# Optimization experiments

Hardware: AMD Instinct MI355X
Metric: run time of the kernel (lower is better)

## Reference

```python
import jax, jax.numpy as jnp
import numpy as np

B, N, DIM, HEADS = 8, 512, 512, 16
MAX_DIST, NG = 128, 32
RBF_STOP = 20.0
EPS = 1e-5


def _ln(x, g, b):
    m = jnp.mean(x, axis=-1, keepdims=True)
    v = jnp.mean((x - m) ** 2, axis=-1, keepdims=True)
    return (x - m) * jax.lax.rsqrt(v + EPS) * g + b


def setup_inputs() -> dict:
    key = jax.random.key(0)
    ks = jax.random.split(key, 12)
    d = DIM
    s = 0.02
    return {
        "x": jax.random.normal(ks[0], (B * N, d), jnp.float32),
        "dist_matrix": jax.random.randint(ks[1], (B, N, N), 0, MAX_DIST, jnp.int32),
        "dist_3d": jax.random.uniform(ks[2], (B, N, N), jnp.float32) * RBF_STOP,
        "norm1_g": jnp.ones((d,), jnp.float32),
        "norm1_b": jnp.zeros((d,), jnp.float32),
        "in_proj_w": jax.random.normal(ks[3], (3 * d, d), jnp.float32) * s,
        "in_proj_b": jnp.zeros((3 * d,), jnp.float32),
        "out_proj_w": jax.random.normal(ks[4], (d, d), jnp.float32) * s,
        "out_proj_b": jnp.zeros((d,), jnp.float32),
        "dist_emb": jax.random.normal(ks[5], (MAX_DIST, HEADS), jnp.float32) * s,
        "rbf_w": jax.random.normal(ks[6], (HEADS, NG), jnp.float32) * s,
        "rbf_b": jnp.zeros((HEADS,), jnp.float32),
        "norm2_g": jnp.ones((d,), jnp.float32),
        "norm2_b": jnp.zeros((d,), jnp.float32),
        "ffn_w1": jax.random.normal(ks[7], (4 * d, d), jnp.float32) * s,
        "ffn_b1": jnp.zeros((4 * d,), jnp.float32),
        "ffn_w2": jax.random.normal(ks[8], (d, 4 * d), jnp.float32) * s,
        "ffn_b2": jnp.zeros((d,), jnp.float32),
        "batch": jnp.repeat(jnp.arange(B, dtype=jnp.int32), N),
    }


def reference(x, dist_matrix, dist_3d, norm1_g, norm1_b, in_proj_w, in_proj_b,
              out_proj_w, out_proj_b, dist_emb, rbf_w, rbf_b, norm2_g, norm2_b,
              ffn_w1, ffn_b1, ffn_w2, ffn_b2, batch):
    b, n = dist_matrix.shape[0], dist_matrix.shape[1]
    d = x.shape[-1]
    dh = d // HEADS
    # equal-size graphs -> to_dense_batch is a reshape, mask all-true
    xd = x.reshape(b, n, d)

    # additive attention bias: shortest-path-distance embedding + RBF projection
    dc = jnp.clip(dist_matrix, 0, MAX_DIST - 1)
    bias_spd = dist_emb[dc]                                  # [b, n, n, H]
    offset = jnp.linspace(0.0, RBF_STOP, NG, dtype=jnp.float32)
    coeff = -0.5 / (RBF_STOP / (NG - 1)) ** 2
    rbf = jnp.exp(coeff * (dist_3d[..., None] - offset) ** 2)  # [b, n, n, NG]
    bias_3d = rbf @ rbf_w.T + rbf_b                          # [b, n, n, H]
    bias = jnp.transpose(bias_spd + bias_3d, (0, 3, 1, 2))   # [b, H, n, n]

    # multi-head attention (pre-norm residual, as in source)
    h = _ln(xd, norm1_g, norm1_b)
    qkv = h @ in_proj_w.T + in_proj_b
    q, k, v = jnp.split(qkv, 3, axis=-1)
    q = q.reshape(b, n, HEADS, dh).transpose(0, 2, 1, 3)
    k = k.reshape(b, n, HEADS, dh).transpose(0, 2, 1, 3)
    v = v.reshape(b, n, HEADS, dh).transpose(0, 2, 1, 3)
    scores = jnp.einsum('bhqd,bhkd->bhqk', q, k) / jnp.sqrt(jnp.float32(dh)) + bias
    attn = jax.nn.softmax(scores, axis=-1)
    ctx = jnp.einsum('bhqk,bhkd->bhqd', attn, v)
    ctx = ctx.transpose(0, 2, 1, 3).reshape(b, n, d)
    attn_out = ctx @ out_proj_w.T + out_proj_b
    h = h + attn_out

    # FFN (dropout inactive at eval)
    h2 = _ln(h, norm2_g, norm2_b)
    ff = jax.nn.gelu(h2 @ ffn_w1.T + ffn_b1, approximate=False) @ ffn_w2.T + ffn_b2
    h = h + ff
    return h.reshape(b * n, d)
```

## Files before the change

### kernel.cpp

```cpp
#include <hip/hip_runtime.h>
#include <hip/hip_bf16.h>
#include <math.h>

#define BB 8
#define NN 512
#define DD 512
#define NH 16
#define DH 32
#define TD 1536
#define NG 32
#define MAXD 128

typedef __attribute__((ext_vector_type(8))) short bf16x8;
typedef __attribute__((ext_vector_type(4))) float f32x4;

__device__ inline short f2bf(float x) {
    __hip_bfloat16 h = __float2bfloat16(x);
    return *reinterpret_cast<short*>(&h);
}
__device__ inline float bf2f(short x) {
    union { unsigned u; float f; } c;
    c.u = ((unsigned)(unsigned short)x) << 16;
    return c.f;
}

__device__ inline void gld_lds16(const void* g, void* l) {
    __builtin_amdgcn_global_load_lds(
        (const __attribute__((address_space(1))) unsigned int*)g,
        (__attribute__((address_space(3))) unsigned int*)l, 16, 0, 0);
}

__global__ __launch_bounds__(256) void cvt_weights(
    const float* __restrict__ s0, const float* __restrict__ s1,
    const float* __restrict__ s2, const float* __restrict__ s3,
    short* __restrict__ d0, short* __restrict__ d1,
    short* __restrict__ d2, short* __restrict__ d3,
    const float* __restrict__ rbfw, const float* __restrict__ rbfb,
    short* __restrict__ Tg,
    int n0, int n1, int n2, int n3) {
    if (blockIdx.y == 4) {
        if (blockIdx.x != 0) return;
        const float STEP  = 20.0f / 31.0f;
        const float COEFF = -0.5f / (STEP * STEP);
        for (int idx = threadIdx.x; idx < 130 * 16; idx += 256) {
            const int i = idx >> 4, h = idx & 15;
            const float x = fminf((float)i, 128.0f) * (20.0f / 128.0f);
            float acc = rbfb[h];
#pragma unroll
            for (int g = 0; g < NG; g++) {
                const float t = x - (float)g * STEP;
                acc += __expf(COEFF * t * t) * rbfw[h * NG + g];
            }
            Tg[idx] = f2bf(acc);
        }
        return;
    }
    const float* s; short* d; int n;
    switch (blockIdx.y) {
        case 0: s = s0; d = d0; n = n0; break;
        case 1: s = s1; d = d1; n = n1; break;
        case 2: s = s2; d = d2; n = n2; break;
        default: s = s3; d = d3; n = n3; break;
    }
    const int i = (blockIdx.x * 256 + threadIdx.x) * 4;
    if (i >= n) return;
    const float4 v = *(const float4*)(s + i);
    short4 o;
    o.x = f2bf(v.x); o.y = f2bf(v.y); o.z = f2bf(v.z); o.w = f2bf(v.w);
    *(short4*)(d + i) = o;
}

__global__ __launch_bounds__(256) void ln_kernel(const float* __restrict__ x,
                                                 const float* __restrict__ g,
                                                 const float* __restrict__ b,
                                                 short* __restrict__ out_bf,
                                                 float* __restrict__ out_f) {
    const int row = blockIdx.x;
    const int tid = threadIdx.x;
    const int wave = tid >> 6, lane = tid & 63;
    const float* xr = x + (size_t)row * DD;
    const float v0 = xr[tid], v1 = xr[tid + 256];
    float s = v0 + v1, q = v0 * v0 + v1 * v1;
#pragma unroll
    for (int m = 1; m < 64; m <<= 1) { s += __shfl_xor(s, m); q += __shfl_xor(q, m); }
    __shared__ float ps[8];
    if (lane == 0) { ps[wave] = s; ps[wave + 4] = q; }
    __syncthreads();
    s = ps[0] + ps[1] + ps[2] + ps[3];
    q = ps[4] + ps[5] + ps[6] + ps[7];
    const float mean = s * (1.0f / DD);
    const float var  = q * (1.0f / DD) - mean * mean;
    const float rs   = rsqrtf(var + 1e-5f);
    const float o0 = (v0 - mean) * rs * g[tid] + b[tid];
    const float o1 = (v1 - mean) * rs * g[tid + 256] + b[tid + 256];
    out_bf[(size_t)row * DD + tid]       = f2bf(o0);
    out_bf[(size_t)row * DD + tid + 256] = f2bf(o1);
    if (out_f) {
        out_f[(size_t)row * DD + tid]       = o0;
        out_f[(size_t)row * DD + tid + 256] = o1;
    }
}

template <int TM, bool GELU, bool RES, int OUT>
__global__ __launch_bounds__(256) void gemm_bf16(
    const short* __restrict__ A, const short* __restrict__ Bw,
    const float* __restrict__ bias, const float* __restrict__ res,
    void* __restrict__ Cout, int M, int Nout, int K) {
    const int MI = TM / 32;
    const int bm = blockIdx.y * TM;
    const int bn = blockIdx.x * 128;
    const int tid  = threadIdx.x;
    const int wave = tid >> 6;
    const int lane = tid & 63;
    const int l16  = lane & 15;
    const int quad = lane >> 4;
    const int wr = (wave >> 1) * (TM / 2);
    const int wc = (wave & 1) * 64;

    __shared__ short As[2][TM * 32];
    __shared__ short Bs[2][128 * 32];

    f32x4 acc[MI][4];
#pragma unroll
    for (int i = 0; i < MI; i++)
#pragma unroll
        for (int j = 0; j < 4; j++) acc[i][j] = (f32x4){0.f, 0.f, 0.f, 0.f};

    auto stage = [&](int buf, int k0) {
        const short* Ab = A + (size_t)bm * K + k0;
        const short* Bb = Bw + (size_t)bn * K + k0;
#pragma unroll
        for (int j = 0; j < TM / 64; j++) {
            const int idx = j * 256 + wave * 64 + lane;
            gld_lds16(Ab + (size_t)(idx >> 2) * K + (idx & 3) * 8,
                      &As[buf][(size_t)(j * 256 + wave * 64) * 8]);
        }
#pragma unroll
        for (int j = 0; j < 2; j++) {
            const int idx = j * 256 + wave * 64 + lane;
            gld_lds16(Bb + (size_t)(idx >> 2) * K + (idx & 3) * 8,
                      &Bs[buf][(size_t)(j * 256 + wave * 64) * 8]);
        }
    };
    auto compute = [&](int buf) {
        bf16x8 af[MI], bfr[4];
#pragma unroll
        for (int i = 0; i < MI; i++)
            af[i] = *(const bf16x8*)&As[buf][(wr + i * 16 + l16) * 32 + quad * 8];
#pragma unroll
        for (int j = 0; j < 4; j++)
            bfr[j] = *(const bf16x8*)&Bs[buf][(wc + j * 16 + l16) * 32 + quad * 8];
#pragma unroll
        for (int i = 0; i < MI; i++)
#pragma unroll
            for (int j = 0; j < 4; j++)
                acc[i][j] = __builtin_amdgcn_mfma_f32_16x16x32_bf16(af[i], bfr[j], acc[i][j], 0, 0, 0);
    };

    stage(0, 0);
    __syncthreads();
    int cur = 0;
    for (int k0 = 32; k0 < K; k0 += 32) {
        stage(cur ^ 1, k0);
        compute(cur);
        __syncthreads();
        cur ^= 1;
    }
    compute(cur);

#pragma unroll
    for (int i = 0; i < MI; i++) {
#pragma unroll
        for (int r = 0; r < 4; r++) {
            const int row = bm + wr + i * 16 + quad * 4 + r;
#pragma unroll
            for (int j = 0; j < 4; j++) {
                const int col = bn + wc + j * 16 + l16;
                float v = acc[i][j][r] + bias[col];
                if (GELU) v = 0.5f * v * (1.0f + erff(v * 0.70710678118654752f));
                if (RES)  v += res[(size_t)row * Nout + col];
                if (OUT == 1) ((short*)Cout)[(size_t)row * Nout + col] = f2bf(v);
                else          ((float*)Cout)[(size_t)row * Nout + col] = v;
            }
        }
    }
}

__global__ __launch_bounds__(512) void attn_mfma(
    const short* __restrict__ qkv,
    const int* __restrict__ dist,
    const float* __restrict__ dist3d,
    const float* __restrict__ demb,
    const short* __restrict__ Tg,
    float* __restrict__ O_part,
    float* __restrict__ l_part)
{
    const int blk  = blockIdx.x;
    const int b    = blk & 7;
    const int t3   = blk >> 3;
    const int part = t3 % 3;
    const int q0   = (t3 / 3) * 16;
    const int tid  = threadIdx.x;
    const int wave = tid >> 6;
    const int lane = tid & 63;
    const int l16  = lane & 15;
    const int quad = lane >> 4;

    __shared__ short Kc[NH * 16 * 32];
    __shared__ short Vc[NH * 16 * 32];
    __shared__ short Pb[8 * 16 * 34];
    __shared__ short Tt[130 * 18];
    __shared__ short Db[128 * 18];

    for (int i = tid; i < 8 * 16 * 34; i += 512) Pb[i] = 0;
    for (int i = tid; i < 130 * 16; i += 512) Tt[(i >> 4) * 18 + (i & 15)] = Tg[i];
    for (int i = tid; i < 128 * 16; i += 512) Db[(i >> 4) * 18 + (i & 15)] = f2bf(demb[i]);

    const float scale = 0.17677669529663687f;
    bf16x8 qf[2];
#pragma unroll
    for (int h = 0; h < 2; h++) {
        const int hh = wave * 2 + h;
        qf[h] = *(const bf16x8*)(qkv + (size_t)(b * NN + q0 + l16) * TD + hh * DH + quad * 8);
    }

    f32x4 O[2][2];
    float lsum[2][4];
#pragma unroll
    for (int h = 0; h < 2; h++) {
#pragma unroll
        for (int tt = 0; tt < 2; tt++) O[h][tt] = (f32x4){0.f, 0.f, 0.f, 0.f};
#pragma unroll
        for (int r = 0; r < 4; r++) lsum[h][r] = 0.f;
    }

    const int cbeg = part * 11;
    const int cend = (part == 2) ? 32 : cbeg + 11;

    for (int c = cbeg; c < cend; c++) {
        const int k0 = c * 16;
        __syncthreads();
#pragma unroll
        for (int l = 0; l < 4; l++) {
            const int idxb = l * 512 + wave * 64;
            const int idx  = idxb + lane;
            const int kk2  = idx & 1023;
            const int h = kk2 >> 6, k = (kk2 >> 2) & 15, c4 = kk2 & 3;
            const short* src = qkv + (size_t)(b * NN + k0 + k) * TD +
                               DD * (1 + (l >> 1)) + h * 32 + c4 * 8;
            short* dstb = (l < 2 ? (short*)Kc : (short*)Vc) + (size_t)(idxb & 1023) * 8;
            gld_lds16(src, dstb);
        }
        float biasr[2][4];
        {
            const int hh0 = wave * 2, hh1 = hh0 + 1;
#pragma unroll
            for (int r = 0; r < 4; r++) {
                const size_t off = ((size_t)(b * NN) + q0 + quad * 4 + r) * NN + k0 + l16;
                int dc = dist[off];
                dc = min(max(dc, 0), MAXD - 1);
                const float x = dist3d[off] * 6.4f;
                int ii = (int)x; ii = min(ii, 127);
                const float fr = x - (float)ii;
                const float t00 = bf2f(Tt[ii * 18 + hh0]), t01 = bf2f(Tt[ii * 18 + 18 + hh0]);
                const float t10 = bf2f(Tt[ii * 18 + hh1]), t11 = bf2f(Tt[ii * 18 + 18 + hh1]);
                biasr[0][r] = bf2f(Db[dc * 18 + hh0]) + t00 + (t01 - t00) * fr;
                biasr[1][r] = bf2f(Db[dc * 18 + hh1]) + t10 + (t11 - t10) * fr;
            }
        }
        __syncthreads();
#pragma unroll
        for (int h = 0; h < 2; h++) {
            const int hh = wave * 2 + h;
            const bf16x8 kf = *(const bf16x8*)&Kc[hh * 512 + l16 * 32 + quad * 8];
            f32x4 s = __builtin_amdgcn_mfma_f32_16x16x32_bf16(
                qf[h], kf, (f32x4){0.f, 0.f, 0.f, 0.f}, 0, 0, 0);
            float pv[4];
#pragma unroll
            for (int r = 0; r < 4; r++) {
                float sv = s[r] * scale + biasr[h][r];
                sv = fminf(sv, 20.f);
                pv[r] = __expf(sv);
                lsum[h][r] += pv[r];
                Pb[wave * 544 + (quad * 4 + r) * 34 + l16] = f2bf(pv[r]);
            }
            const bf16x8 pf = *(const bf16x8*)&Pb[wave * 544 + l16 * 34 + quad * 8];
#pragma unroll
            for (int tt = 0; tt < 2; tt++) {
                bf16x8 vf;
                if (quad < 2) {
#pragma unroll
                    for (int j = 0; j < 8; j++)
                        vf[j] = Vc[hh * 512 + (quad * 8 + j) * 32 + tt * 16 + l16];
                } else {
#pragma unroll
                    for (int j = 0; j < 8; j++) vf[j] = 0;
                }
                O[h][tt] = __builtin_amdgcn_mfma_f32_16x16x32_bf16(pf, vf, O[h][tt], 0, 0, 0);
            }
        }
    }
    const size_t poff = (size_t)part * 4096;
#pragma unroll
    for (int h = 0; h < 2; h++) {
        const int hh = wave * 2 + h;
#pragma unroll
        for (int m = 1; m < 16; m <<= 1)
#pragma unroll
            for (int r = 0; r < 4; r++) lsum[h][r] += __shfl_xor(lsum[h][r], m);
#pragma unroll
        for (int r = 0; r < 4; r++) {
            const size_t row = (size_t)(b * NN + q0 + quad * 4 + r);
#pragma unroll
            for (int tt = 0; tt < 2; tt++)
                O_part[(poff + row) * DD + hh * DH + tt * 16 + l16] = O[h][tt][r];
            if (l16 == 0) l_part[(poff + row) * NH + hh] = lsum[h][r];
        }
    }
}

__global__ __launch_bounds__(256) void attn_combine(
    const float* __restrict__ O_part, const float* __restrict__ l_part,
    short* __restrict__ ctx) {
    const int e = (blockIdx.x * 256 + threadIdx.x) * 4;
    const int row = e >> 9, d = e & 511, h = d >> 5;
    const size_t PO = (size_t)4096 * 512;
    const float4 o0 = *(const float4*)(O_part + e);
    const float4 o1 = *(const float4*)(O_part + PO + e);
    const float4 o2 = *(const float4*)(O_part + 2 * PO + e);
    const int li = row * NH + h;
    const float l = l_part[li] + l_part[4096 * NH + li] + l_part[2 * 4096 * NH + li];
    const float rinv = 1.0f / l;
    short4 o;
    o.x = f2bf((o0.x + o1.x + o2.x) * rinv);
    o.y = f2bf((o0.y + o1.y + o2.y) * rinv);
    o.z = f2bf((o0.z + o1.z + o2.z) * rinv);
    o.w = f2bf((o0.w + o1.w + o2.w) * rinv);
    *(short4*)(ctx + e) = o;
}

extern "C" void kernel_launch(void* const* d_in, const int* in_sizes, int n_in,
                              void* d_out, int out_size, void* d_ws, size_t ws_size,
                              hipStream_t stream) {
    const float* x      = (const float*)d_in[0];
    const int*   dist   = (const int*)d_in[1];
    const float* dist3d = (const float*)d_in[2];
    const float* n1g    = (const float*)d_in[3];
    const float* n1b    = (const float*)d_in[4];
    const float* win    = (const float*)d_in[5];
    const float* bin    = (const float*)d_in[6];
    const float* wo     = (const float*)d_in[7];
    const float* bo     = (const float*)d_in[8];
    const float* demb   = (const float*)d_in[9];
    const float* rbfw   = (const float*)d_in[10];
    const float* rbfb   = (const float*)d_in[11];
    const float* n2g    = (const float*)d_in[12];
    const float* n2b    = (const float*)d_in[13];
    const float* w1     = (const float*)d_in[14];
    const float* b1     = (const float*)d_in[15];
    const float* w2     = (const float*)d_in[16];
    const float* b2     = (const float*)d_in[17];

    char* p = (char*)d_ws;
    short* h_bf   = (short*)p; p += (size_t)4096 * 512 * 2;
    float* h_f    = (float*)p; p += (size_t)4096 * 512 * 4;
    short* qkv_bf = (short*)p; p += (size_t)4096 * 1536 * 2;
    short* ctx_bf = (short*)p; p += (size_t)4096 * 512 * 2;
    float* hres   = (float*)p; p += (size_t)4096 * 512 * 4;
    short* h2_bf  = (short*)p; p += (size_t)4096 * 512 * 2;
    short* win_bf = (short*)p; p += (size_t)1536 * 512 * 2;
    short* wo_bf  = (short*)p; p += (size_t)512 * 512 * 2;
    short* w1_bf  = (short*)p; p += (size_t)2048 * 512 * 2;
    short* w2_bf  = (short*)p; p += (size_t)512 * 2048 * 2;
    short* Tg     = (short*)p; p += (size_t)8192;
    float* O_part = (float*)p;
    short* mid_bf = (short*)p;
    p += (size_t)3 * 4096 * 512 * 4;
    float* l_part = (float*)p; p += (size_t)3 * 4096 * 16 * 4;

    const int M = BB * NN;

    cvt_weights<<<dim3(1024, 5), 256, 0, stream>>>(
        win, wo, w1, w2, win_bf, wo_bf, w1_bf, w2_bf, rbfw, rbfb, Tg,
        1536 * 512, 512 * 512, 2048 * 512, 512 * 2048);
    ln_kernel<<<M, 256, 0, stream>>>(x, n1g, n1b, h_bf, h_f);
    gemm_bf16<64, false, false, 1><<<dim3(12, 64), 256, 0, stream>>>(
        h_bf, win_bf, bin, nullptr, qkv_bf, M, TD, DD);
    attn_mfma<<<768, 512, 0, stream>>>(
        qkv_bf, dist, dist3d, demb, Tg, O_part, l_part);
    attn_combine<<<2048, 256, 0, stream>>>(O_part, l_part, ctx_bf);
    gemm_bf16<64, false, true, 0><<<dim3(4, 64), 256, 0, stream>>>(
        ctx_bf, wo_bf, bo, h_f, hres, M, DD, DD);
    ln_kernel<<<M, 256, 0, stream>>>(hres, n2g, n2b, h2_bf, nullptr);
    gemm_bf16<64, true, false, 1><<<dim3(16, 64), 256, 0, stream>>>(
        h2_bf, w1_bf, b1, nullptr, mid_bf, M, 2048, DD);
    gemm_bf16<64, false, true, 0><<<dim3(4, 64), 256, 0, stream>>>(
        mid_bf, w2_bf, b2, hres, (float*)d_out, M, DD, 2048);
}
```

Measured before the change: 262.2 us.

## Fuse attention combine into out-proj GEMM, use bf16 partials, retile GEMMs

Removes the separate attn_combine kernel: the out-projection GEMM now sums the three bf16 partial outputs and normalizes them by the summed softmax denominators while staging A tiles. Attention partial outputs become bf16 instead of fp32, the residual is read from the bf16 LN output instead of a stored fp32 copy, and the QKV and FFN1 GEMMs move to 128-row tiles. The attention loop swaps block barriers for per-wave waitcnt since each wave now loads only its own heads' K/V, and the Pb padding is removed. These changes cut memory traffic and launches, but add bf16 rounding on the partials and residual, and the removed padding may cause LDS bank conflicts.

```diff
diff --git a/kernel.cpp b/kernel.cpp
--- a/kernel.cpp
+++ b/kernel.cpp
@@ -73,8 +73,7 @@
 __global__ __launch_bounds__(256) void ln_kernel(const float* __restrict__ x,
                                                  const float* __restrict__ g,
                                                  const float* __restrict__ b,
-                                                 short* __restrict__ out_bf,
-                                                 float* __restrict__ out_f) {
+                                                 short* __restrict__ out_bf) {
     const int row = blockIdx.x;
     const int tid = threadIdx.x;
     const int wave = tid >> 6, lane = tid & 63;
@@ -91,17 +90,11 @@
     const float mean = s * (1.0f / DD);
     const float var  = q * (1.0f / DD) - mean * mean;
     const float rs   = rsqrtf(var + 1e-5f);
-    const float o0 = (v0 - mean) * rs * g[tid] + b[tid];
-    const float o1 = (v1 - mean) * rs * g[tid + 256] + b[tid + 256];
-    out_bf[(size_t)row * DD + tid]       = f2bf(o0);
-    out_bf[(size_t)row * DD + tid + 256] = f2bf(o1);
-    if (out_f) {
-        out_f[(size_t)row * DD + tid]       = o0;
-        out_f[(size_t)row * DD + tid + 256] = o1;
-    }
-}
-
-template <int TM, bool GELU, bool RES, int OUT>
+    out_bf[(size_t)row * DD + tid]       = f2bf((v0 - mean) * rs * g[tid] + b[tid]);
+    out_bf[(size_t)row * DD + tid + 256] = f2bf((v1 - mean) * rs * g[tid + 256] + b[tid + 256]);
+}
+
+template <int TM, bool GELU, bool RES, bool OUTBF>
 __global__ __launch_bounds__(256) void gemm_bf16(
     const short* __restrict__ A, const short* __restrict__ Bw,
     const float* __restrict__ bias, const float* __restrict__ res,
@@ -179,8 +172,109 @@
                 float v = acc[i][j][r] + bias[col];
                 if (GELU) v = 0.5f * v * (1.0f + erff(v * 0.70710678118654752f));
                 if (RES)  v += res[(size_t)row * Nout + col];
-                if (OUT == 1) ((short*)Cout)[(size_t)row * Nout + col] = f2bf(v);
-                else          ((float*)Cout)[(size_t)row * Nout + col] = v;
+                if (OUTBF) ((short*)Cout)[(size_t)row * Nout + col] = f2bf(v);
+                else       ((float*)Cout)[(size_t)row * Nout + col] = v;
+            }
+        }
+    }
+}
+
+__global__ __launch_bounds__(256) void gemm_op(
+    const short* __restrict__ Opart,
+    const float* __restrict__ lpart,
+    const short* __restrict__ Bw,
+    const float* __restrict__ bias,
+    const short* __restrict__ resb,
+    float* __restrict__ Cout) {
+    const int bm = blockIdx.y * 64;
+    const int bn = blockIdx.x * 128;
+    const int tid  = threadIdx.x;
+    const int wave = tid >> 6;
+    const int lane = tid & 63;
+    const int l16  = lane & 15;
+    const int quad = lane >> 4;
+    const int wr = (wave >> 1) * 32;
+    const int wc = (wave & 1) * 64;
+    const size_t PO = (size_t)4096 * 512;
+
+    __shared__ short As[2][64 * 32];
+    __shared__ short Bs[2][128 * 32];
+    __shared__ float Lr[64 * 16];
+
+    for (int i = tid; i < 64 * 16; i += 256) {
+        const int idx = (bm + (i >> 4)) * 16 + (i & 15);
+        Lr[i] = 1.0f / (lpart[idx] + lpart[4096 * 16 + idx] + lpart[2 * 4096 * 16 + idx]);
+    }
+    __syncthreads();
+
+    f32x4 acc[2][4];
+#pragma unroll
+    for (int i = 0; i < 2; i++)
+#pragma unroll
+        for (int j = 0; j < 4; j++) acc[i][j] = (f32x4){0.f, 0.f, 0.f, 0.f};
+
+    const int arow = tid >> 2;
+    const int acb  = (tid & 3) * 8;
+
+    auto stageA = [&](int buf, int k0) {
+        const size_t base = (size_t)(bm + arow) * 512 + k0 + acb;
+        const bf16x8 a0 = *(const bf16x8*)(Opart + base);
+        const bf16x8 a1 = *(const bf16x8*)(Opart + PO + base);
+        const bf16x8 a2 = *(const bf16x8*)(Opart + 2 * PO + base);
+        const float rv = Lr[arow * 16 + (k0 >> 5)];
+        bf16x8 o;
+#pragma unroll
+        for (int e = 0; e < 8; e++)
+            o[e] = f2bf((bf2f(a0[e]) + bf2f(a1[e]) + bf2f(a2[e])) * rv);
+        *(bf16x8*)&As[buf][arow * 32 + acb] = o;
+    };
+    auto stageB = [&](int buf, int k0) {
+        const short* Bb = Bw + (size_t)bn * 512 + k0;
+#pragma unroll
+        for (int j = 0; j < 2; j++) {
+            const int idx = j * 256 + wave * 64 + lane;
+            gld_lds16(Bb + (size_t)(idx >> 2) * 512 + (idx & 3) * 8,
+                      &Bs[buf][(size_t)(j * 256 + wave * 64) * 8]);
+        }
+    };
+    auto compute = [&](int buf) {
+        bf16x8 af[2], bfr[4];
+#pragma unroll
+        for (int i = 0; i < 2; i++)
+            af[i] = *(const bf16x8*)&As[buf][(wr + i * 16 + l16) * 32 + quad * 8];
+#pragma unroll
+        for (int j = 0; j < 4; j++)
+            bfr[j] = *(const bf16x8*)&Bs[buf][(wc + j * 16 + l16) * 32 + quad * 8];
+#pragma unroll
+        for (int i = 0; i < 2; i++)
+#pragma unroll
+            for (int j = 0; j < 4; j++)
+                acc[i][j] = __builtin_amdgcn_mfma_f32_16x16x32_bf16(af[i], bfr[j], acc[i][j], 0, 0, 0);
+    };
+
+    stageB(0, 0);
+    stageA(0, 0);
+    __syncthreads();
+    int cur = 0;
+    for (int k0 = 32; k0 < 512; k0 += 32) {
+        stageB(cur ^ 1, k0);
+        stageA(cur ^ 1, k0);
+        compute(cur);
+        __syncthreads();
+        cur ^= 1;
+    }
+    compute(cur);
+
+#pragma unroll
+    for (int i = 0; i < 2; i++) {
+#pragma unroll
+        for (int r = 0; r < 4; r++) {
+            const int row = bm + wr + i * 16 + quad * 4 + r;
+#pragma unroll
+            for (int j = 0; j < 4; j++) {
+                const int col = bn + wc + j * 16 + l16;
+                float v = acc[i][j][r] + bias[col] + bf2f(resb[(size_t)row * 512 + col]);
+                Cout[(size_t)row * 512 + col] = v;
             }
         }
     }
@@ -192,7 +286,7 @@
     const float* __restrict__ dist3d,
     const float* __restrict__ demb,
     const short* __restrict__ Tg,
-    float* __restrict__ O_part,
+    short* __restrict__ O_part,
     float* __restrict__ l_part)
 {
     const int blk  = blockIdx.x;
@@ -208,11 +302,11 @@
 
     __shared__ short Kc[NH * 16 * 32];
     __shared__ short Vc[NH * 16 * 32];
-    __shared__ short Pb[8 * 16 * 34];
+    __shared__ short Pb[8 * 16 * 32];
     __shared__ short Tt[130 * 18];
     __shared__ short Db[128 * 18];
 
-    for (int i = tid; i < 8 * 16 * 34; i += 512) Pb[i] = 0;
+    for (int i = tid; i < 8 * 16 * 32; i += 512) Pb[i] = 0;
     for (int i = tid; i < 130 * 16; i += 512) Tt[(i >> 4) * 18 + (i & 15)] = Tg[i];
     for (int i = tid; i < 128 * 16; i += 512) Db[(i >> 4) * 18 + (i & 15)] = f2bf(demb[i]);
 
@@ -234,22 +328,22 @@
         for (int r = 0; r < 4; r++) lsum[h][r] = 0.f;
     }
 
+    __syncthreads();
+
     const int cbeg = part * 11;
     const int cend = (part == 2) ? 32 : cbeg + 11;
 
+    const int sk = lane >> 2;
+    const int sc = lane & 3;
+
     for (int c = cbeg; c < cend; c++) {
         const int k0 = c * 16;
-        __syncthreads();
-#pragma unroll
-        for (int l = 0; l < 4; l++) {
-            const int idxb = l * 512 + wave * 64;
-            const int idx  = idxb + lane;
-            const int kk2  = idx & 1023;
-            const int h = kk2 >> 6, k = (kk2 >> 2) & 15, c4 = kk2 & 3;
-            const short* src = qkv + (size_t)(b * NN + k0 + k) * TD +
-                               DD * (1 + (l >> 1)) + h * 32 + c4 * 8;
-            short* dstb = (l < 2 ? (short*)Kc : (short*)Vc) + (size_t)(idxb & 1023) * 8;
-            gld_lds16(src, dstb);
+        const size_t rowb = (size_t)(b * NN + k0 + sk) * TD + sc * 8;
+#pragma unroll
+        for (int h = 0; h < 2; h++) {
+            const int hh = wave * 2 + h;
+            gld_lds16(qkv + rowb + DD + hh * DH,     &Kc[hh * 512]);
+            gld_lds16(qkv + rowb + 2 * DD + hh * DH, &Vc[hh * 512]);
         }
         float biasr[2][4];
         {
@@ -268,7 +362,9 @@
                 biasr[1][r] = bf2f(Db[dc * 18 + hh1]) + t10 + (t11 - t10) * fr;
             }
         }
-        __syncthreads();
+        asm volatile("" ::: "memory");
+        __builtin_amdgcn_s_waitcnt(0x0F70);
+        asm volatile("" ::: "memory");
 #pragma unroll
         for (int h = 0; h < 2; h++) {
             const int hh = wave * 2 + h;
@@ -282,9 +378,9 @@
                 sv = fminf(sv, 20.f);
                 pv[r] = __expf(sv);
                 lsum[h][r] += pv[r];
-                Pb[wave * 544 + (quad * 4 + r) * 34 + l16] = f2bf(pv[r]);
-            }
-            const bf16x8 pf = *(const bf16x8*)&Pb[wave * 544 + l16 * 34 + quad * 8];
+                Pb[wave * 512 + (quad * 4 + r) * 32 + l16] = f2bf(pv[r]);
+            }
+            const bf16x8 pf = *(const bf16x8*)&Pb[wave * 512 + l16 * 32 + quad * 8];
 #pragma unroll
             for (int tt = 0; tt < 2; tt++) {
                 bf16x8 vf;
@@ -299,6 +395,9 @@
                 O[h][tt] = __builtin_amdgcn_mfma_f32_16x16x32_bf16(pf, vf, O[h][tt], 0, 0, 0);
             }
         }
+        asm volatile("" ::: "memory");
+        __builtin_amdgcn_s_waitcnt(0xC07F);
+        asm volatile("" ::: "memory");
     }
     const size_t poff = (size_t)part * 4096;
 #pragma unroll
@@ -313,30 +412,10 @@
             const size_t row = (size_t)(b * NN + q0 + quad * 4 + r);
 #pragma unroll
             for (int tt = 0; tt < 2; tt++)
-                O_part[(poff + row) * DD + hh * DH + tt * 16 + l16] = O[h][tt][r];
+                O_part[(poff + row) * DD + hh * DH + tt * 16 + l16] = f2bf(O[h][tt][r]);
             if (l16 == 0) l_part[(poff + row) * NH + hh] = lsum[h][r];
         }
     }
-}
-
-__global__ __launch_bounds__(256) void attn_combine(
-    const float* __restrict__ O_part, const float* __restrict__ l_part,
-    short* __restrict__ ctx) {
-    const int e = (blockIdx.x * 256 + threadIdx.x) * 4;
-    const int row = e >> 9, d = e & 511, h = d >> 5;
-    const size_t PO = (size_t)4096 * 512;
-    const float4 o0 = *(const float4*)(O_part + e);
-    const float4 o1 = *(const float4*)(O_part + PO + e);
-    const float4 o2 = *(const float4*)(O_part + 2 * PO + e);
-    const int li = row * NH + h;
-    const float l = l_part[li] + l_part[4096 * NH + li] + l_part[2 * 4096 * NH + li];
-    const float rinv = 1.0f / l;
-    short4 o;
-    o.x = f2bf((o0.x + o1.x + o2.x) * rinv);
-    o.y = f2bf((o0.y + o1.y + o2.y) * rinv);
-    o.z = f2bf((o0.z + o1.z + o2.z) * rinv);
-    o.w = f2bf((o0.w + o1.w + o2.w) * rinv);
-    *(short4*)(ctx + e) = o;
 }
 
 extern "C" void kernel_launch(void* const* d_in, const int* in_sizes, int n_in,
@@ -363,9 +442,7 @@
 
     char* p = (char*)d_ws;
     short* h_bf   = (short*)p; p += (size_t)4096 * 512 * 2;
-    float* h_f    = (float*)p; p += (size_t)4096 * 512 * 4;
     short* qkv_bf = (short*)p; p += (size_t)4096 * 1536 * 2;
-    short* ctx_bf = (short*)p; p += (size_t)4096 * 512 * 2;
     float* hres   = (float*)p; p += (size_t)4096 * 512 * 4;
     short* h2_bf  = (short*)p; p += (size_t)4096 * 512 * 2;
     short* win_bf = (short*)p; p += (size_t)1536 * 512 * 2;
@@ -373,9 +450,9 @@
     short* w1_bf  = (short*)p; p += (size_t)2048 * 512 * 2;
     short* w2_bf  = (short*)p; p += (size_t)512 * 2048 * 2;
     short* Tg     = (short*)p; p += (size_t)8192;
-    float* O_part = (float*)p;
+    short* O_part = (short*)p;
     short* mid_bf = (short*)p;
-    p += (size_t)3 * 4096 * 512 * 4;
+    p += (size_t)4096 * 2048 * 2;
     float* l_part = (float*)p; p += (size_t)3 * 4096 * 16 * 4;
 
     const int M = BB * NN;
@@ -383,17 +460,16 @@
     cvt_weights<<<dim3(1024, 5), 256, 0, stream>>>(
         win, wo, w1, w2, win_bf, wo_bf, w1_bf, w2_bf, rbfw, rbfb, Tg,
         1536 * 512, 512 * 512, 2048 * 512, 512 * 2048);
-    ln_kernel<<<M, 256, 0, stream>>>(x, n1g, n1b, h_bf, h_f);
-    gemm_bf16<64, false, false, 1><<<dim3(12, 64), 256, 0, stream>>>(
+    ln_kernel<<<M, 256, 0, stream>>>(x, n1g, n1b, h_bf);
+    gemm_bf16<128, false, false, true><<<dim3(12, 32), 256, 0, stream>>>(
         h_bf, win_bf, bin, nullptr, qkv_bf, M, TD, DD);
     attn_mfma<<<768, 512, 0, stream>>>(
         qkv_bf, dist, dist3d, demb, Tg, O_part, l_part);
-    attn_combine<<<2048, 256, 0, stream>>>(O_part, l_part, ctx_bf);
-    gemm_bf16<64, false, true, 0><<<dim3(4, 64), 256, 0, stream>>>(
-        ctx_bf, wo_bf, bo, h_f, hres, M, DD, DD);
-    ln_kernel<<<M, 256, 0, stream>>>(hres, n2g, n2b, h2_bf, nullptr);
-    gemm_bf16<64, true, false, 1><<<dim3(16, 64), 256, 0, stream>>>(
+    gemm_op<<<dim3(4, 64), 256, 0, stream>>>(
+        O_part, l_part, wo_bf, bo, h_bf, hres);
+    ln_kernel<<<M, 256, 0, stream>>>(hres, n2g, n2b, h2_bf);
+    gemm_bf16<128, true, false, true><<<dim3(16, 32), 256, 0, stream>>>(
         h2_bf, w1_bf, b1, nullptr, mid_bf, M, 2048, DD);
-    gemm_bf16<64, false, true, 0><<<dim3(4, 64), 256, 0, stream>>>(
+    gemm_bf16<64, false, true, false><<<dim3(4, 64), 256, 0, stream>>>(
         mid_bf, w2_bf, b2, hres, (float*)d_out, M, DD, 2048);
 }
```

Result: no change. 257.6 us (-1.7%).
